# Kernel optimization log

Hardware: AMD Instinct MI355X
Metric: run time of the kernel (lower is better)

Reference implementation:

```python
import jax, jax.numpy as jnp
import numpy as np

N_NODES = 100000


def gcn_conv(x, W, b, src, dst, n_nodes):
    """PyG GCNConv: add self-loops, symmetric D^-1/2 A D^-1/2 normalization,
    linear transform, gather-scale-scatter aggregation, bias."""
    h = x @ W  # [N, out]
    loops = jnp.arange(n_nodes, dtype=src.dtype)
    s = jnp.concatenate([src, loops])  # sources incl. self-loops
    d = jnp.concatenate([dst, loops])  # targets incl. self-loops
    deg = jax.ops.segment_sum(jnp.ones_like(d, dtype=h.dtype), d,
                              num_segments=n_nodes)  # in-degree (+1 self loop)
    dinv = jnp.where(deg > 0, jax.lax.rsqrt(deg), 0.0)
    norm = dinv[s] * dinv[d]  # [E+N]
    msg = h[s] * norm[:, None]  # gather + scale  [E+N, out]
    out = jax.ops.segment_sum(msg, d, num_segments=n_nodes)  # scatter-add
    return out + b


def setup_inputs() -> dict:
    key = jax.random.key(0)
    k1, k2, k3, k4, k5, k6 = jax.random.split(key, 6)
    in_ch, out_ch = 128, 64
    n_edges = 1_600_000
    x = jax.random.normal(k1, (N_NODES, in_ch), dtype=jnp.float32)
    edge_index = jax.random.randint(k2, (2, n_edges), 0, N_NODES, dtype=jnp.int64)
    # Glorot-style init for GCN weights, zero bias (PyG defaults)
    W_enc = jax.random.normal(k3, (in_ch, out_ch), dtype=jnp.float32) * (1.0 / np.sqrt(in_ch))
    b_enc = jnp.zeros((out_ch,), dtype=jnp.float32)
    W_dec = jax.random.normal(k4, (out_ch, in_ch), dtype=jnp.float32) * (1.0 / np.sqrt(out_ch))
    b_dec = jnp.zeros((in_ch,), dtype=jnp.float32)
    return {"x": x, "edge_index": edge_index,
            "W_enc": W_enc, "b_enc": b_enc, "W_dec": W_dec, "b_dec": b_dec}


def reference(x, edge_index, W_enc, b_enc, W_dec, b_dec):
    src, dst = edge_index[0], edge_index[1]
    loc_emb = gcn_conv(x, W_enc, b_enc, src, dst, N_NODES)
    loc_reconstruct = gcn_conv(loc_emb, W_dec, b_dec, src, dst, N_NODES)
    return (loc_emb, loc_reconstruct)
```

## Files before the change

kernel.cpp:

```cpp
#include <hip/hip_runtime.h>
#include <hip/hip_fp16.h>


#define BSHIFT 7
#define BNODES (1 << BSHIFT)
#define NB_LDS 1024

__global__ __launch_bounds__(1024)
void part_kernel(const int* __restrict__ src, const int* __restrict__ dst,
                 int E, int NB, int* __restrict__ gcur, int* __restrict__ gbuf,
                 int BSTRIDE)
{
    __shared__ int hist[NB_LDS];
    __shared__ int bbase[NB_LDS];
    const int tid = threadIdx.x;
    for (int i = tid; i < NB; i += 1024) hist[i] = 0;
    __syncthreads();

    const int base = (blockIdx.x * 1024 + tid) * 4;
    int bk[4], lp[4], pk[4];
    int nv = 0;
    if (base + 4 <= E) {
        const int4 d4 = *reinterpret_cast<const int4*>(dst + base);
        const int4 s4 = *reinterpret_cast<const int4*>(src + base);
        nv = 4;
        #pragma unroll
        for (int k = 0; k < 4; ++k) {
            const int d = (&d4.x)[k];
            bk[k] = d >> BSHIFT;
            pk[k] = ((&s4.x)[k] << BSHIFT) | (d & (BNODES - 1));
            lp[k] = atomicAdd(&hist[bk[k]], 1);
        }
    } else {
        for (int k = 0; base + k < E && k < 4; ++k) {
            const int d = dst[base + k];
            bk[nv] = d >> BSHIFT;
            pk[nv] = (src[base + k] << BSHIFT) | (d & (BNODES - 1));
            lp[nv] = atomicAdd(&hist[bk[nv]], 1);
            ++nv;
        }
    }
    __syncthreads();
    for (int i = tid; i < NB; i += 1024) {
        const int c = hist[i];
        bbase[i] = c ? atomicAdd(&gcur[i], c) : 0;
    }
    __syncthreads();
    for (int k = 0; k < nv; ++k) {
        const int pos = bbase[bk[k]] + lp[k];
        if (pos < BSTRIDE) gbuf[(size_t)bk[k] * BSTRIDE + pos] = pk[k];
    }
}

__global__ __launch_bounds__(256)
void csr_kernel(const int* __restrict__ gcur, const int* __restrict__ gbuf,
                int BSTRIDE, int* __restrict__ csr, int cap,
                int* __restrict__ cnt, float* __restrict__ dinv, int M)
{
    __shared__ int cur[BNODES];
    const int tid = threadIdx.x;
    const int b   = blockIdx.x;
    if (tid < BNODES) cur[tid] = 0;
    __syncthreads();

    int nb = gcur[b];
    if (nb > BSTRIDE) nb = BSTRIDE;
    const int* __restrict__ buf = gbuf + (size_t)b * BSTRIDE;
    const int n0 = b << BSHIFT;

    for (int i = tid; i < nb; i += 256) {
        const int p = buf[i];
        const int d = p & (BNODES - 1);
        const int s = p >> BSHIFT;
        const int lpos = atomicAdd(&cur[d], 1);
        if (lpos < cap) csr[(size_t)(n0 + d) * cap + lpos] = s;
    }
    __syncthreads();
    const int n = n0 + tid;
    if (tid < BNODES && n < M) {
        const int c = cur[tid];
        cnt[n]  = c;
        dinv[n] = rsqrtf((float)c + 1.0f);
    }
}

template<int K, int N, int CG, int R, bool HOUT>
__global__ __launch_bounds__(256)
void gemm_rb(const float* __restrict__ X, const float* __restrict__ W,
             const float* __restrict__ dinv, const float* __restrict__ bias,
             float* __restrict__ out, __half* __restrict__ outh, int M)
{
    constexpr int RG = 256 / CG;
    constexpr int TM = RG * R;
    __shared__ float Ws[K * N];

    const int tid = threadIdx.x;
    for (int i = tid; i < K * N / 4; i += 256)
        reinterpret_cast<float4*>(Ws)[i] = reinterpret_cast<const float4*>(W)[i];
    __syncthreads();

    const int cg   = tid % CG;
    const int rg   = tid / CG;
    const int c0   = cg * 8;
    const int row0 = blockIdx.x * TM + rg * R;

    float acc[R][8];
    #pragma unroll
    for (int r = 0; r < R; ++r)
        #pragma unroll
        for (int c = 0; c < 8; ++c) acc[r][c] = 0.f;

    const float* xp[R];
    #pragma unroll
    for (int r = 0; r < R; ++r) {
        int rr = row0 + r;
        if (rr >= M) rr = M - 1;
        xp[r] = X + (size_t)rr * K;
    }

    float4 xv[R];
    #pragma unroll
    for (int r = 0; r < R; ++r) xv[r] = *reinterpret_cast<const float4*>(xp[r]);

    for (int k = 0; k < K; k += 4) {
        float4 xn[R];
        const bool more = (k + 4 < K);
        if (more) {
            #pragma unroll
            for (int r = 0; r < R; ++r)
                xn[r] = *reinterpret_cast<const float4*>(xp[r] + k + 4);
        }
        #pragma unroll
        for (int kk = 0; kk < 4; ++kk) {
            const float4 w0 = *reinterpret_cast<const float4*>(&Ws[(k + kk) * N + c0]);
            const float4 w1 = *reinterpret_cast<const float4*>(&Ws[(k + kk) * N + c0 + 4]);
            #pragma unroll
            for (int r = 0; r < R; ++r) {
                const float xs = (&xv[r].x)[kk];
                acc[r][0] += xs * w0.x; acc[r][1] += xs * w0.y;
                acc[r][2] += xs * w0.z; acc[r][3] += xs * w0.w;
                acc[r][4] += xs * w1.x; acc[r][5] += xs * w1.y;
                acc[r][6] += xs * w1.z; acc[r][7] += xs * w1.w;
            }
        }
        if (more) {
            #pragma unroll
            for (int r = 0; r < R; ++r) xv[r] = xn[r];
        }
    }

    float4 bv0 = make_float4(0.f, 0.f, 0.f, 0.f);
    float4 bv1 = make_float4(0.f, 0.f, 0.f, 0.f);
    if (bias) {
        bv0 = *reinterpret_cast<const float4*>(&bias[c0]);
        bv1 = *reinterpret_cast<const float4*>(&bias[c0 + 4]);
    }

    #pragma unroll
    for (int r = 0; r < R; ++r) {
        const int gr = row0 + r;
        if (gr < M) {
            const float d = dinv[gr];
            if constexpr (HOUT) {
                union { __half2 h2[4]; uint4 u; } pk;
                pk.h2[0] = __floats2half2_rn(acc[r][0] * d, acc[r][1] * d);
                pk.h2[1] = __floats2half2_rn(acc[r][2] * d, acc[r][3] * d);
                pk.h2[2] = __floats2half2_rn(acc[r][4] * d, acc[r][5] * d);
                pk.h2[3] = __floats2half2_rn(acc[r][6] * d, acc[r][7] * d);
                *reinterpret_cast<uint4*>(&outh[(size_t)gr * N + c0]) = pk.u;
            } else {
                float4 v0, v1;
                v0.x = acc[r][0] * d + bv0.x; v0.y = acc[r][1] * d + bv0.y;
                v0.z = acc[r][2] * d + bv0.z; v0.w = acc[r][3] * d + bv0.w;
                v1.x = acc[r][4] * d + bv1.x; v1.y = acc[r][5] * d + bv1.y;
                v1.z = acc[r][6] * d + bv1.z; v1.w = acc[r][7] * d + bv1.w;
                *reinterpret_cast<float4*>(&out[(size_t)gr * N + c0])     = v0;
                *reinterpret_cast<float4*>(&out[(size_t)gr * N + c0 + 4]) = v1;
            }
        }
    }
}

template<bool FIRST>
__global__ __launch_bounds__(256)
void gcn_agg(const __half* __restrict__ hsh, const int* __restrict__ csr,
             const int* __restrict__ cnt, const float* __restrict__ dinv,
             const float* __restrict__ bias, float* __restrict__ outf,
             __half* __restrict__ outh, int M, int cap)
{
    const int lane = threadIdx.x & 63;
    int n = (blockIdx.x * 256 + threadIdx.x) >> 6;
    if (n >= M) return;
    n = __builtin_amdgcn_readfirstlane(n);
    int deg = cnt[n];
    if (deg > cap) deg = cap;
    const int* __restrict__ lst = csr + (size_t)n * cap;

    float acc = __half2float(hsh[(size_t)n * 64 + lane]);

    int j = 0;
    for (; j + 16 <= deg; j += 16) {
        int   s[16];
        float v[16];
        #pragma unroll
        for (int k = 0; k < 16; ++k) s[k] = lst[j + k];
        #pragma unroll
        for (int k = 0; k < 16; ++k) v[k] = __half2float(hsh[(size_t)s[k] * 64 + lane]);
        float t = 0.f;
        #pragma unroll
        for (int k = 0; k < 16; ++k) t += v[k];
        acc += t;
    }
    for (; j + 4 <= deg; j += 4) {
        const int s0 = lst[j], s1 = lst[j + 1], s2 = lst[j + 2], s3 = lst[j + 3];
        const float v0 = __half2float(hsh[(size_t)s0 * 64 + lane]);
        const float v1 = __half2float(hsh[(size_t)s1 * 64 + lane]);
        const float v2 = __half2float(hsh[(size_t)s2 * 64 + lane]);
        const float v3 = __half2float(hsh[(size_t)s3 * 64 + lane]);
        acc += (v0 + v1) + (v2 + v3);
    }
    for (; j < deg; ++j) acc += __half2float(hsh[(size_t)lst[j] * 64 + lane]);

    if constexpr (FIRST) {
        const float dv = dinv[n];
        const float e  = acc * dv + bias[lane];
        outf[(size_t)n * 64 + lane] = e;
        outh[(size_t)n * 64 + lane] = __float2half_rn(e * dv);
    } else {
        outf[(size_t)n * 64 + lane] = acc;
    }
}

extern "C" void kernel_launch(void* const* d_in, const int* in_sizes, int n_in,
                              void* d_out, int out_size, void* d_ws, size_t ws_size,
                              hipStream_t stream)
{
    const float* x    = (const float*)d_in[0];
    const int*   ei   = (const int*)  d_in[1];
    const float* Wenc = (const float*)d_in[2];
    const float* benc = (const float*)d_in[3];
    const float* Wdec = (const float*)d_in[4];
    const float* bdec = (const float*)d_in[5];

    const int M = in_sizes[0] / 128;
    const int E = in_sizes[1] / 2;
    const int* src  = ei;
    const int* dstv = ei + E;

    float* emb   = (float*)d_out;
    float* recon = (float*)d_out + (size_t)M * 64;

    const int NB      = (M + BNODES - 1) >> BSHIFT;
    const int BSTRIDE = 3072;

    __half* hs1h  = (__half*)d_ws;
    __half* ghalf = (__half*)((int*)d_ws + (size_t)M * 32);
    int*    gbuf  = (int*)d_ws + (size_t)M * 64;
    float*  agg2  = (float*)((int*)d_ws + (size_t)M * 64);
    int*    cnt   = (int*)d_ws + (size_t)M * 128;
    float*  dinv  = (float*)((int*)d_ws + (size_t)M * 129);
    int*    gcur  = (int*)d_ws + (size_t)M * 130;
    int*    csr   = (int*)d_ws + (size_t)M * 130 + 1024;

    const size_t used = ((size_t)M * 130 + 1024) * 4;
    int cap = 64;
    const size_t avail = (ws_size > used) ? (ws_size - used) / ((size_t)M * 4) : 0;
    if ((size_t)cap > avail) cap = (int)avail;

    hipMemsetAsync(gcur, 0, 1024 * sizeof(int), stream);

    part_kernel<<<(E + 4095) / 4096, 1024, 0, stream>>>(src, dstv, E, NB, gcur, gbuf, BSTRIDE);
    csr_kernel<<<NB, 256, 0, stream>>>(gcur, gbuf, BSTRIDE, csr, cap, cnt, dinv, M);

    const int aggBlocks = (M + 3) / 4;

    gemm_rb<128, 64, 8, 4, true><<<(M + 127) / 128, 256, 0, stream>>>(
        x, Wenc, dinv, nullptr, nullptr, hs1h, M);
    gcn_agg<true><<<aggBlocks, 256, 0, stream>>>(
        hs1h, csr, cnt, dinv, benc, emb, ghalf, M, cap);

    gcn_agg<false><<<aggBlocks, 256, 0, stream>>>(
        ghalf, csr, cnt, nullptr, nullptr, agg2, nullptr, M, cap);
    gemm_rb<64, 128, 16, 4, false><<<(M + 63) / 64, 256, 0, stream>>>(
        agg2, Wdec, dinv, bdec, recon, nullptr, M);
}
```

Baseline: 292.1 us.

## Fuse second-layer aggregation with decoder GEMM in one kernel

Replaces the separate second aggregation kernel and decoder GEMM with a single kernel. Each wavefront aggregates 8 nodes' 64-wide features into registers, stages them in LDS, and multiplies by Wdec held in LDS to write the 128-wide output directly. This removes the fp32 agg2 intermediate write and read-back and one launch. In exchange, every block reloads the whole 32KB Wdec into LDS, the LDS footprint limits occupancy, and the gather loop runs serially over 8 nodes per wave. The bias load in gemm_rb also moves into the non-half branch.

Measured after the change: 313.3 us. +7.3%, slower.

```diff
diff --git a/kernel.cpp b/kernel.cpp
--- a/kernel.cpp
+++ b/kernel.cpp
@@ -147,13 +147,6 @@
             #pragma unroll
             for (int r = 0; r < R; ++r) xv[r] = xn[r];
         }
-    }
-
-    float4 bv0 = make_float4(0.f, 0.f, 0.f, 0.f);
-    float4 bv1 = make_float4(0.f, 0.f, 0.f, 0.f);
-    if (bias) {
-        bv0 = *reinterpret_cast<const float4*>(&bias[c0]);
-        bv1 = *reinterpret_cast<const float4*>(&bias[c0 + 4]);
     }
 
     #pragma unroll
@@ -169,6 +162,8 @@
                 pk.h2[3] = __floats2half2_rn(acc[r][6] * d, acc[r][7] * d);
                 *reinterpret_cast<uint4*>(&outh[(size_t)gr * N + c0]) = pk.u;
             } else {
+                float4 bv0 = *reinterpret_cast<const float4*>(&bias[c0]);
+                float4 bv1 = *reinterpret_cast<const float4*>(&bias[c0 + 4]);
                 float4 v0, v1;
                 v0.x = acc[r][0] * d + bv0.x; v0.y = acc[r][1] * d + bv0.y;
                 v0.z = acc[r][2] * d + bv0.z; v0.w = acc[r][3] * d + bv0.w;
@@ -181,12 +176,11 @@
     }
 }
 
-template<bool FIRST>
 __global__ __launch_bounds__(256)
-void gcn_agg(const __half* __restrict__ hsh, const int* __restrict__ csr,
-             const int* __restrict__ cnt, const float* __restrict__ dinv,
-             const float* __restrict__ bias, float* __restrict__ outf,
-             __half* __restrict__ outh, int M, int cap)
+void gcn_agg1(const __half* __restrict__ hsh, const int* __restrict__ csr,
+              const int* __restrict__ cnt, const float* __restrict__ dinv,
+              const float* __restrict__ bias, float* __restrict__ outf,
+              __half* __restrict__ outh, int M, int cap)
 {
     const int lane = threadIdx.x & 63;
     int n = (blockIdx.x * 256 + threadIdx.x) >> 6;
@@ -221,13 +215,106 @@
     }
     for (; j < deg; ++j) acc += __half2float(hsh[(size_t)lst[j] * 64 + lane]);
 
-    if constexpr (FIRST) {
-        const float dv = dinv[n];
-        const float e  = acc * dv + bias[lane];
-        outf[(size_t)n * 64 + lane] = e;
-        outh[(size_t)n * 64 + lane] = __float2half_rn(e * dv);
-    } else {
-        outf[(size_t)n * 64 + lane] = acc;
+    const float dv = dinv[n];
+    const float e  = acc * dv + bias[lane];
+    outf[(size_t)n * 64 + lane] = e;
+    outh[(size_t)n * 64 + lane] = __float2half_rn(e * dv);
+}
+
+__global__ __launch_bounds__(256)
+void agg2_dec(const __half* __restrict__ ghalf, const int* __restrict__ csr,
+              const int* __restrict__ cnt, const float* __restrict__ dinv,
+              const float* __restrict__ Wdec, const float* __restrict__ bdec,
+              float* __restrict__ recon, int M, int cap)
+{
+    __shared__ float Wl[64 * 128];
+    __shared__ float accb[4][64][8];
+
+    const int tid  = threadIdx.x;
+    const int lane = tid & 63;
+    const int wid  = tid >> 6;
+
+    for (int i = tid; i < 64 * 128 / 4; i += 256)
+        reinterpret_cast<float4*>(Wl)[i] = reinterpret_cast<const float4*>(Wdec)[i];
+    __syncthreads();
+
+    const int nbase = (blockIdx.x * 4 + wid) * 8;
+
+    float acc[8];
+    #pragma unroll
+    for (int i = 0; i < 8; ++i) {
+        int n = nbase + i;
+        if (n >= M) n = M - 1;
+        n = __builtin_amdgcn_readfirstlane(n);
+        int deg = cnt[n];
+        if (deg > cap) deg = cap;
+        const int* __restrict__ lst = csr + (size_t)n * cap;
+
+        float a = __half2float(ghalf[(size_t)n * 64 + lane]);
+        int j = 0;
+        for (; j + 16 <= deg; j += 16) {
+            int   s[16];
+            float v[16];
+            #pragma unroll
+            for (int k = 0; k < 16; ++k) s[k] = lst[j + k];
+            #pragma unroll
+            for (int k = 0; k < 16; ++k) v[k] = __half2float(ghalf[(size_t)s[k] * 64 + lane]);
+            float t = 0.f;
+            #pragma unroll
+            for (int k = 0; k < 16; ++k) t += v[k];
+            a += t;
+        }
+        for (; j + 4 <= deg; j += 4) {
+            const int s0 = lst[j], s1 = lst[j + 1], s2 = lst[j + 2], s3 = lst[j + 3];
+            const float v0 = __half2float(ghalf[(size_t)s0 * 64 + lane]);
+            const float v1 = __half2float(ghalf[(size_t)s1 * 64 + lane]);
+            const float v2 = __half2float(ghalf[(size_t)s2 * 64 + lane]);
+            const float v3 = __half2float(ghalf[(size_t)s3 * 64 + lane]);
+            a += (v0 + v1) + (v2 + v3);
+        }
+        for (; j < deg; ++j) a += __half2float(ghalf[(size_t)lst[j] * 64 + lane]);
+        acc[i] = a;
+    }
+
+    {
+        float4 t0 = make_float4(acc[0], acc[1], acc[2], acc[3]);
+        float4 t1 = make_float4(acc[4], acc[5], acc[6], acc[7]);
+        *reinterpret_cast<float4*>(&accb[wid][lane][0]) = t0;
+        *reinterpret_cast<float4*>(&accb[wid][lane][4]) = t1;
+    }
+    asm volatile("s_waitcnt lgkmcnt(0)" ::: "memory");
+    __builtin_amdgcn_sched_barrier(0);
+
+    float p0[8], p1[8];
+    #pragma unroll
+    for (int i = 0; i < 8; ++i) { p0[i] = 0.f; p1[i] = 0.f; }
+
+    #pragma unroll 4
+    for (int k = 0; k < 64; ++k) {
+        const float2 wv = *reinterpret_cast<const float2*>(&Wl[k * 128 + lane * 2]);
+        const float4 a0 = *reinterpret_cast<const float4*>(&accb[wid][k][0]);
+        const float4 a1 = *reinterpret_cast<const float4*>(&accb[wid][k][4]);
+        p0[0] += a0.x * wv.x; p1[0] += a0.x * wv.y;
+        p0[1] += a0.y * wv.x; p1[1] += a0.y * wv.y;
+        p0[2] += a0.z * wv.x; p1[2] += a0.z * wv.y;
+        p0[3] += a0.w * wv.x; p1[3] += a0.w * wv.y;
+        p0[4] += a1.x * wv.x; p1[4] += a1.x * wv.y;
+        p0[5] += a1.y * wv.x; p1[5] += a1.y * wv.y;
+        p0[6] += a1.z * wv.x; p1[6] += a1.z * wv.y;
+        p0[7] += a1.w * wv.x; p1[7] += a1.w * wv.y;
+    }
+
+    const float2 b2 = reinterpret_cast<const float2*>(bdec)[lane];
+    #pragma unroll
+    for (int i = 0; i < 8; ++i) {
+        const int n = nbase + i;
+        if (n < M) {
+            const float dv = dinv[n];
+            float2 o;
+            o.x = p0[i] * dv + b2.x;
+            o.y = p1[i] * dv + b2.y;
+            *reinterpret_cast<float2*>(&recon[(size_t)n * 128 + lane * 2]) = o;
+        }
     }
 }
 
@@ -256,7 +343,6 @@
     __half* hs1h  = (__half*)d_ws;
     __half* ghalf = (__half*)((int*)d_ws + (size_t)M * 32);
     int*    gbuf  = (int*)d_ws + (size_t)M * 64;
-    float*  agg2  = (float*)((int*)d_ws + (size_t)M * 64);
     int*    cnt   = (int*)d_ws + (size_t)M * 128;
     float*  dinv  = (float*)((int*)d_ws + (size_t)M * 129);
     int*    gcur  = (int*)d_ws + (size_t)M * 130;
@@ -272,15 +358,11 @@
     part_kernel<<<(E + 4095) / 4096, 1024, 0, stream>>>(src, dstv, E, NB, gcur, gbuf, BSTRIDE);
     csr_kernel<<<NB, 256, 0, stream>>>(gcur, gbuf, BSTRIDE, csr, cap, cnt, dinv, M);
 
-    const int aggBlocks = (M + 3) / 4;
-
     gemm_rb<128, 64, 8, 4, true><<<(M + 127) / 128, 256, 0, stream>>>(
         x, Wenc, dinv, nullptr, nullptr, hs1h, M);
-    gcn_agg<true><<<aggBlocks, 256, 0, stream>>>(
+    gcn_agg1<<<(M + 3) / 4, 256, 0, stream>>>(
         hs1h, csr, cnt, dinv, benc, emb, ghalf, M, cap);
 
-    gcn_agg<false><<<aggBlocks, 256, 0, stream>>>(
-        ghalf, csr, cnt, nullptr, nullptr, agg2, nullptr, M, cap);
-    gemm_rb<64, 128, 16, 4, false><<<(M + 63) / 64, 256, 0, stream>>>(
-        agg2, Wdec, dinv, bdec, recon, nullptr, M);
-}
+    agg2_dec<<<(M + 31) / 32, 256, 0, stream>>>(
+        ghalf, csr, cnt, dinv, Wdec, bdec, recon, M, cap);
+}
```
